# Performance work log

Hardware: AMD Instinct MI355X
Metric: run time of the kernel (lower is better)

## Reference

```python
import jax, jax.numpy as jnp
import numpy as np

B, CIN, L = 4, 128, 2048
D_MODEL, D_STATE, EXPAND, HEADDIM, NGROUPS = 256, 16, 3, 3, 1
D_INNER = EXPAND * D_MODEL            # 768
NHEADS = D_INNER // HEADDIM           # 256
CONV_DIM = D_INNER + 2 * NGROUPS * D_STATE   # 800
D_IN_PROJ = 2 * D_INNER + 2 * NGROUPS * D_STATE + NHEADS  # 1824
K_PROJ, D_CONV = 4, 4
EPS = 1e-5


def setup_inputs() -> dict:
    key = jax.random.key(0)
    ks = jax.random.split(key, 9)
    x = jax.random.normal(ks[0], (B, CIN, L), jnp.float32)
    proj_w = jax.random.normal(ks[1], (D_MODEL, CIN, K_PROJ), jnp.float32) / np.float32(np.sqrt(CIN * K_PROJ))
    in_proj_w = jax.random.normal(ks[2], (D_IN_PROJ, D_MODEL), jnp.float32) / np.float32(np.sqrt(D_MODEL))
    conv_w = jax.random.normal(ks[3], (CONV_DIM, 1, D_CONV), jnp.float32) / np.float32(np.sqrt(D_CONV))
    conv_b = jax.random.normal(ks[4], (CONV_DIM,), jnp.float32) * 0.01
    # dt_bias = inverse-softplus of dt ~ LogUniform[1e-3, 1e-1] (mamba2 init)
    u = jax.random.uniform(ks[5], (NHEADS,), jnp.float32)
    dt = jnp.exp(u * np.float32(np.log(0.1) - np.log(1e-3)) + np.float32(np.log(1e-3)))
    dt_bias = dt + jnp.log(-jnp.expm1(-dt))
    A_log = jnp.log(1.0 + 15.0 * jax.random.uniform(ks[6], (NHEADS,), jnp.float32))  # A in [-16,-1]
    D_skip = jnp.ones((NHEADS,), jnp.float32)
    norm_w = jnp.ones((D_INNER,), jnp.float32)
    out_proj_w = jax.random.normal(ks[7], (D_MODEL, D_INNER), jnp.float32) / np.float32(np.sqrt(D_INNER))
    return {"x": x, "proj_w": proj_w, "in_proj_w": in_proj_w, "conv_w": conv_w,
            "conv_b": conv_b, "dt_bias": dt_bias, "A_log": A_log, "D_skip": D_skip,
            "norm_w": norm_w, "out_proj_w": out_proj_w}


def _forward(x, proj_w, in_proj_w, conv_w, conv_b, dt_bias, A_log, D_skip, norm_w, out_proj_w):
    # outer Conv1d, padding='same' (k=4 -> left 1, right 2), no bias: (B,CIN,L)->(B,D_MODEL,L)
    h = jax.lax.conv_general_dilated(x, proj_w, (1,), [(1, 2)],
                                     dimension_numbers=("NCH", "OIH", "NCH"))
    u = h.transpose(0, 2, 1)                          # (B, L, d_model)
    zxbcdt = jnp.einsum("bld,ed->ble", u, in_proj_w)  # (B, L, 1824)
    z = zxbcdt[..., :D_INNER]                                     # (B,L,768)
    xBC = zxbcdt[..., D_INNER:D_INNER + CONV_DIM]                 # (B,L,800)
    dt = zxbcdt[..., D_INNER + CONV_DIM:]                         # (B,L,256)
    dt = jax.nn.softplus(dt + dt_bias)
    # depthwise causal conv (pad d_conv-1 on left) + SiLU
    xBC_c = jax.lax.conv_general_dilated(xBC.transpose(0, 2, 1), conv_w, (1,), [(D_CONV - 1, 0)],
                                         feature_group_count=CONV_DIM,
                                         dimension_numbers=("NCH", "OIH", "NCH"))
    xBC = jax.nn.silu(xBC_c + conv_b[None, :, None]).transpose(0, 2, 1)  # (B,L,800)
    xs = xBC[..., :D_INNER].reshape(B, L, NHEADS, HEADDIM)        # (B,L,H,P)
    Bm = xBC[..., D_INNER:D_INNER + D_STATE]                      # (B,L,N) (ngroups=1)
    Cm = xBC[..., D_INNER + D_STATE:]                             # (B,L,N)
    A = -jnp.exp(A_log)                                           # (H,)

    def step(hst, inp):
        dt_t, x_t, B_t, C_t = inp                 # (B,H),(B,H,P),(B,N),(B,N)
        dA = jnp.exp(dt_t * A)[:, :, None, None]  # (B,H,1,1)
        hst = dA * hst + jnp.einsum("bh,bhp,bn->bhpn", dt_t, x_t, B_t)
        y_t = jnp.einsum("bhpn,bn->bhp", hst, C_t)
        return hst, y_t

    h0 = jnp.zeros((B, NHEADS, HEADDIM, D_STATE), x.dtype)
    _, ys = jax.lax.scan(step, h0, (dt.transpose(1, 0, 2), xs.transpose(1, 0, 2, 3),
                                    Bm.transpose(1, 0, 2), Cm.transpose(1, 0, 2)))
    y = ys.transpose(1, 0, 2, 3) + D_skip[None, None, :, None] * xs   # (B,L,H,P)
    y = y.reshape(B, L, D_INNER)
    # gated RMSNorm: gate first, then normalize (norm_before_gate=False)
    y = y * jax.nn.silu(z)
    y = y * jax.lax.rsqrt(jnp.mean(y * y, axis=-1, keepdims=True) + EPS) * norm_w
    out = jnp.einsum("ble,de->bld", y, out_proj_w)   # (B,L,d_model)
    return out.transpose(0, 2, 1)                    # (B,d_model,L)


def reference(x, proj_w, in_proj_w, conv_w, conv_b, dt_bias, A_log, D_skip, norm_w, out_proj_w):
    return _forward(x, proj_w, in_proj_w, conv_w, conv_b, dt_bias, A_log, D_skip, norm_w, out_proj_w)
```

## Files before the change

### kernel.cpp

```cpp
#include <hip/hip_runtime.h>
#include <hip/hip_fp16.h>
#include <math.h>

#define B_     4
#define CIN    128
#define LEN    2048
#define DMODEL 256
#define DSTATE 16
#define NHEADS 256
#define DINNER 768
#define CONVDIM 800
#define DINPROJ 1824
#define EPS_   1e-5f
#define BAND   64
#define NBAND  32

typedef _Float16 f16x8 __attribute__((ext_vector_type(8)));
typedef _Float16 f16x4 __attribute__((ext_vector_type(4)));
typedef float    f32x4 __attribute__((ext_vector_type(4)));

__device__ __forceinline__ float silu_(float x){ return x / (1.0f + __expf(-x)); }
__device__ __forceinline__ float softplus_(float x){
    return x > 0.f ? x + log1pf(__expf(-x)) : log1pf(__expf(x));
}

__device__ __forceinline__ void gl2lds16(const _Float16* g, _Float16* l){
    __builtin_amdgcn_global_load_lds(
        (const __attribute__((address_space(1))) void*)g,
        (__attribute__((address_space(3))) void*)l, 16, 0, 0);
}

__global__ __launch_bounds__(256) void k_f2h(const float* __restrict__ a,
                                             _Float16* __restrict__ o, int n){
    for (int i = blockIdx.x * 256 + threadIdx.x; i < n; i += gridDim.x * 256)
        o[i] = (_Float16)a[i];
}

__global__ __launch_bounds__(256) void k_im2col(const float* __restrict__ x,
                                                _Float16* __restrict__ xcol){
    __shared__ float xs[CIN][68];
    int blk = blockIdx.x;
    int b  = blk >> 5;
    int l0 = (blk & 31) << 6;
    const float* xb = x + (size_t)b * CIN * LEN;
    for (int idx = threadIdx.x; idx < CIN * 67; idx += 256){
        int ci = idx / 67, j = idx % 67;
        int gl = l0 - 1 + j;
        xs[ci][j] = (gl >= 0 && gl < LEN) ? xb[ci * LEN + gl] : 0.f;
    }
    __syncthreads();
    #pragma unroll
    for (int v = 0; v < 16; v++){
        int id = v * 256 + threadIdx.x;
        int rl = id >> 6, c = id & 63;
        f16x8 pk;
        #pragma unroll
        for (int e = 0; e < 8; e++){
            int ci = c * 2 + (e >> 2), k = e & 3;
            pk[e] = (_Float16)xs[ci][rl + k];
        }
        *(f16x8*)&xcol[((size_t)(b * LEN + l0 + rl)) * 512 + c * 8] = pk;
    }
}

template<int K, int EPI>
__global__ __launch_bounds__(256) void k_gemm(const _Float16* __restrict__ A,
                                              const _Float16* __restrict__ Bw,
                                              const float* __restrict__ dt_bias,
                                              _Float16* __restrict__ o_u,
                                              _Float16* __restrict__ o_z,
                                              _Float16* __restrict__ o_xbc,
                                              _Float16* __restrict__ o_dt,
                                              float* __restrict__ o_f){
    __shared__ __align__(16) _Float16 As[128 * 32];
    __shared__ __align__(16) _Float16 Bs[128 * 32];
    int tid  = threadIdx.x;
    int wv   = tid >> 6;
    int lane = tid & 63;
    int quad = lane >> 4;
    int l16  = lane & 15;
    int m0 = blockIdx.x * 128;
    int n0 = blockIdx.y * 128;
    int wm = (wv >> 1) * 64;
    int wn = (wv & 1) * 64;
    int srow = lane >> 2;
    int scol = (lane & 3) * 8;

    f32x4 acc[4][4];
    #pragma unroll
    for (int i = 0; i < 4; i++)
        #pragma unroll
        for (int j = 0; j < 4; j++)
            acc[i][j] = (f32x4){0.f, 0.f, 0.f, 0.f};

    for (int k0 = 0; k0 < K; k0 += 32){
        #pragma unroll
        for (int j = 0; j < 2; j++){
            int ar = m0 + wv * 32 + j * 16 + srow;
            gl2lds16(A + (size_t)ar * K + k0 + scol,
                     &As[(wv * 32 + j * 16) * 32]);
            int nr = n0 + wv * 32 + j * 16 + srow;
            if (EPI == 1) nr = nr > (DINPROJ - 1) ? (DINPROJ - 1) : nr;
            gl2lds16(Bw + (size_t)nr * K + k0 + scol,
                     &Bs[(wv * 32 + j * 16) * 32]);
        }
        __syncthreads();
        f16x8 af[4], bf[4];
        #pragma unroll
        for (int i = 0; i < 4; i++)
            af[i] = *(const f16x8*)&As[(wm + i * 16 + l16) * 32 + quad * 8];
        #pragma unroll
        for (int j = 0; j < 4; j++)
            bf[j] = *(const f16x8*)&Bs[(wn + j * 16 + l16) * 32 + quad * 8];
        #pragma unroll
        for (int i = 0; i < 4; i++)
            #pragma unroll
            for (int j = 0; j < 4; j++)
                acc[i][j] = __builtin_amdgcn_mfma_f32_16x16x32_f16(
                                af[i], bf[j], acc[i][j], 0, 0, 0);
        __syncthreads();
    }

    if (EPI == 0){
        #pragma unroll
        for (int j = 0; j < 4; j++){
            int col = n0 + wn + j * 16 + l16;
            #pragma unroll
            for (int i = 0; i < 4; i++){
                int row = m0 + wm + i * 16 + quad * 4;
                #pragma unroll
                for (int r = 0; r < 4; r++)
                    o_u[(size_t)(row + r) * DMODEL + col] = (_Float16)acc[i][j][r];
            }
        }
    } else if (EPI == 1){
        #pragma unroll
        for (int j = 0; j < 4; j++){
            int col = n0 + wn + j * 16 + l16;
            if (col < DINNER){
                #pragma unroll
                for (int i = 0; i < 4; i++){
                    int row = m0 + wm + i * 16 + quad * 4;
                    #pragma unroll
                    for (int r = 0; r < 4; r++)
                        o_z[(size_t)(row + r) * DINNER + col] = (_Float16)acc[i][j][r];
                }
            } else if (col < DINNER + CONVDIM){
                int cc = col - DINNER;
                #pragma unroll
                for (int i = 0; i < 4; i++){
                    int row = m0 + wm + i * 16 + quad * 4;
                    #pragma unroll
                    for (int r = 0; r < 4; r++)
                        o_xbc[(size_t)(row + r) * CONVDIM + cc] = (_Float16)acc[i][j][r];
                }
            } else if (col < DINPROJ){
                int hh = col - (DINNER + CONVDIM);
                float bias = dt_bias[hh];
                #pragma unroll
                for (int i = 0; i < 4; i++){
                    int row = m0 + wm + i * 16 + quad * 4;
                    #pragma unroll
                    for (int r = 0; r < 4; r++)
                        o_dt[(size_t)(row + r) * NHEADS + hh] =
                            (_Float16)softplus_(acc[i][j][r] + bias);
                }
            }
        }
    } else {
        #pragma unroll
        for (int i = 0; i < 4; i++){
            int row = m0 + wm + i * 16 + quad * 4;
            int b = row >> 11, l = row & (LEN - 1);
            #pragma unroll
            for (int j = 0; j < 4; j++){
                int d = n0 + wn + j * 16 + l16;
                *(f32x4*)&o_f[(((size_t)(b * DMODEL + d)) << 11) + l] = acc[i][j];
            }
        }
    }
}

__global__ __launch_bounds__(256) void k_dwconv(const __half* __restrict__ xbc,
                                                const float* __restrict__ cw,
                                                const float* __restrict__ cb,
                                                __half* __restrict__ xcc){
    int idx = blockIdx.x * 256 + threadIdx.x;
    int c = idx % CONVDIM;
    int r = idx / CONVDIM;
    int l = r & (LEN - 1);
    float4 wv = *(const float4*)(cw + c * 4);
    float acc = cb[c];
    if (l >= 3){
        const __half* base = xbc + (size_t)(r - 3) * CONVDIM + c;
        acc += __half2float(base[0]) * wv.x + __half2float(base[CONVDIM]) * wv.y +
               __half2float(base[2 * CONVDIM]) * wv.z + __half2float(base[3 * CONVDIM]) * wv.w;
    } else {
        const float wk[4] = {wv.x, wv.y, wv.z, wv.w};
        for (int k = 0; k < 4; k++){
            int t = l - 3 + k;
            if (t >= 0) acc += __half2float(xbc[(size_t)(r + k - 3) * CONVDIM + c]) * wk[k];
        }
    }
    xcc[idx] = __float2half(silu_(acc));
}

__global__ __launch_bounds__(256, 3) void k_y(const __half* __restrict__ dtb,
                                              const __half* __restrict__ xcc,
                                              const float* __restrict__ A_log,
                                              __half* __restrict__ y,
                                              float* __restrict__ E0,
                                              __half* __restrict__ cstate,
                                              float* __restrict__ dsum){
    __shared__ __align__(16) char smem[45056];
    __half* sBC = (__half*)smem;
    __half* sX  = (__half*)(smem + 5120);
    float*  sG  = (float*)(smem + 18432);
    float*  sD  = (float*)(smem + 22528);
    __half* sDT = (__half*)(smem + 31744);
    __half* sHL = (__half*)(smem + 35840);

    int band = blockIdx.x, hg = blockIdx.y, b = blockIdx.z;
    int row0 = band * BAND;
    int tid = threadIdx.x;
    int wv = tid >> 6, lane = tid & 63;

    {
        int row = tid >> 2, off = tid & 3;
        f16x8 v = *(const f16x8*)((const char*)xcc +
                    (size_t)(b * LEN + row0 + row) * 1600 + 1536 + off * 16);
        *(f16x8*)&sBC[row * 40 + off * 8] = v;
    }
    #pragma unroll
    for (int i = 0; i < 3; i++){
        int c = tid + i * 256;
        int row = c / 12, off = c % 12;
        f16x8 v = *(const f16x8*)((const char*)xcc +
                    (size_t)(b * LEN + row0 + row) * 1600 + hg * 192 + off * 16);
        *(f16x8*)&sX[row * 104 + off * 8] = v;
    }
    gl2lds16((const _Float16*)((const char*)dtb +
               (size_t)(b * LEN + row0 + (tid >> 2)) * 512 + hg * 64 + (lane & 3) * 16),
             (_Float16*)(smem + 31744 + wv * 1024));
    __syncthreads();

    {
        int h = tid & 31;
        float A = -__expf(A_log[hg * 32 + h]);
        #pragma unroll
        for (int i = 0; i < 8; i++){
            int t = (tid >> 5) + i * 8;
            sD[t * 36 + h] = __expf(A * __half2float(sDT[t * 32 + h]));
        }
    }
    __syncthreads();

    if (tid < 32){
        int h = tid;
        float E = 1.f;
        float* ep = E0 + ((size_t)(b * LEN + row0)) * 256 + hg * 32 + h;
        for (int t = 0; t < 64; t++){
            E *= sD[t * 36 + h];
            *ep = E;
            ep += 256;
        }
        dsum[(size_t)(b * 256 + hg * 32 + h) * NBAND + band] = E;
    } else if (tid < 160){
        int base = (tid - 32) * 8;
        int tt = base >> 4;
        f16x8 ca = *(const f16x8*)&sBC[tt * 40 + 16];
        f16x8 cb = *(const f16x8*)&sBC[tt * 40 + 24];
        float cf[16];
        #pragma unroll
        for (int n = 0; n < 16; n++) cf[n] = (n < 8) ? (float)ca[n] : (float)cb[n - 8];
        #pragma unroll
        for (int j = 0; j < 8; j++){
            int idx = base + j;
            int t2 = idx >> 4, ss = idx & 15;
            if (t2 != tt){
                tt = t2;
                ca = *(const f16x8*)&sBC[tt * 40 + 16];
                cb = *(const f16x8*)&sBC[tt * 40 + 24];
                #pragma unroll
                for (int n = 0; n < 16; n++) cf[n] = (n < 8) ? (float)ca[n] : (float)cb[n - 8];
            }
            int s = (tt & 48) + ss;
            f16x8 ba = *(const f16x8*)&sBC[s * 40];
            f16x8 bb = *(const f16x8*)&sBC[s * 40 + 8];
            float acc = 0.f;
            #pragma unroll
            for (int n = 0; n < 8; n++)
                acc += cf[n] * (float)ba[n] + cf[n + 8] * (float)bb[n];
            sG[tt * 16 + ss] = acc;
        }
    } else {
        for (int idx = tid - 160; idx < 2048; idx += 96){
            int t = idx >> 5, h = idx & 31;
            float dtv = __half2float(sDT[t * 32 + h]);
            int xi = t * 104 + h * 3;
            sX[xi]     = (_Float16)((float)sX[xi]     * dtv);
            sX[xi + 1] = (_Float16)((float)sX[xi + 1] * dtv);
            sX[xi + 2] = (_Float16)((float)sX[xi + 2] * dtv);
        }
    }
    __syncthreads();

    int t = tid >> 2, hsub = tid & 3, Hb = hsub * 8;
    int tmod = t & 15, tseg = t & 48;
    float w[8], y0[8], y1[8], y2[8];
    #pragma unroll
    for (int i = 0; i < 8; i++){ w[i] = 1.f; y0[i] = 0.f; y1[i] = 0.f; y2[i] = 0.f; }

    for (int d = 0; d <= tmod; d++){
        int s = t - d;
        float g = sG[t * 16 + (tmod - d)];
        f32x4 Dv0 = *(const f32x4*)&sD[s * 36 + Hb];
        f32x4 Dv1 = *(const f32x4*)&sD[s * 36 + Hb + 4];
        f16x8 xv0 = *(const f16x8*)&sX[s * 104 + hsub * 24];
        f16x8 xv1 = *(const f16x8*)&sX[s * 104 + hsub * 24 + 8];
        f16x8 xv2 = *(const f16x8*)&sX[s * 104 + hsub * 24 + 16];
        #define XV(i) ((i) < 8 ? (float)xv0[(i)] : ((i) < 16 ? (float)xv1[(i)-8] : (float)xv2[(i)-16]))
        #pragma unroll
        for (int hh = 0; hh < 8; hh++){
            float wg = w[hh] * g;
            y0[hh] = fmaf(wg, XV(hh * 3 + 0), y0[hh]);
            y1[hh] = fmaf(wg, XV(hh * 3 + 1), y1[hh]);
            y2[hh] = fmaf(wg, XV(hh * 3 + 2), y2[hh]);
            w[hh] *= (hh < 4) ? Dv0[hh] : Dv1[hh - 4];
        }
        #undef XV
    }

    if (tid < 128){
        int h2 = tid >> 2, ng = tid & 3;
        float hc[12];
        #pragma unroll
        for (int i = 0; i < 12; i++) hc[i] = 0.f;
        for (int k = 0; k < 4; k++){
            float F[12];
            #pragma unroll
            for (int i = 0; i < 12; i++) F[i] = 0.f;
            float v = 1.f;
            for (int ss = 15; ss >= 0; ss--){
                int s = k * 16 + ss;
                float x0 = (float)sX[s * 104 + h2 * 3];
                float x1 = (float)sX[s * 104 + h2 * 3 + 1];
                float x2 = (float)sX[s * 104 + h2 * 3 + 2];
                f16x4 bv = *(const f16x4*)&sBC[s * 40 + ng * 4];
                #pragma unroll
                for (int nn = 0; nn < 4; nn++){
                    float wb = v * (float)bv[nn];
                    F[nn * 3 + 0] = fmaf(wb, x0, F[nn * 3 + 0]);
                    F[nn * 3 + 1] = fmaf(wb, x1, F[nn * 3 + 1]);
                    F[nn * 3 + 2] = fmaf(wb, x2, F[nn * 3 + 2]);
                }
                v *= sD[s * 36 + h2];
            }
            #pragma unroll
            for (int i = 0; i < 12; i++) hc[i] = fmaf(v, hc[i], F[i]);
            if (k < 3){
                __half* hp = &sHL[(k * 32 + h2) * 48 + ng * 12];
                #pragma unroll
                for (int q = 0; q < 3; q++){
                    f16x4 pk;
                    #pragma unroll
                    for (int e = 0; e < 4; e++) pk[e] = (_Float16)hc[q * 4 + e];
                    *(f16x4*)&hp[q * 4] = pk;
                }
            } else {
                __half* cp = cstate + ((size_t)((b * 256 + hg * 32 + h2) * NBAND + band)) * 48 + ng * 12;
                #pragma unroll
                for (int q = 0; q < 3; q++){
                    f16x4 pk;
                    #pragma unroll
                    for (int e = 0; e < 4; e++) pk[e] = (_Float16)hc[q * 4 + e];
                    *(f16x4*)&cp[q * 4] = pk;
                }
            }
        }
    }
    __syncthreads();

    {
        f16x8 cva = *(const f16x8*)&sBC[t * 40 + 16];
        f16x8 cvb = *(const f16x8*)&sBC[t * 40 + 24];
        float cf[16];
        #pragma unroll
        for (int n = 0; n < 16; n++) cf[n] = (n < 8) ? (float)cva[n] : (float)cvb[n - 8];
        int k = t >> 4;
        if (k > 0){
            #pragma unroll
            for (int hh = 0; hh < 8; hh++){
                int h = Hb + hh;
                const __half* hl = &sHL[((k - 1) * 32 + h) * 48];
                f16x8 hv0 = *(const f16x8*)&hl[0];
                f16x8 hv1 = *(const f16x8*)&hl[8];
                f16x8 hv2 = *(const f16x8*)&hl[16];
                f16x8 hv3 = *(const f16x8*)&hl[24];
                f16x8 hv4 = *(const f16x8*)&hl[32];
                f16x8 hv5 = *(const f16x8*)&hl[40];
                #define HV(i) ((i)<8?(float)hv0[(i)]:(i)<16?(float)hv1[(i)-8]:(i)<24?(float)hv2[(i)-16]:\
                               (i)<32?(float)hv3[(i)-24]:(i)<40?(float)hv4[(i)-32]:(float)hv5[(i)-40])
                float a0 = 0.f, a1 = 0.f, a2 = 0.f;
                #pragma unroll
                for (int n = 0; n < 16; n++){
                    a0 = fmaf(cf[n], HV(n * 3 + 0), a0);
                    a1 = fmaf(cf[n], HV(n * 3 + 1), a1);
                    a2 = fmaf(cf[n], HV(n * 3 + 2), a2);
                }
                #undef HV
                y0[hh] = fmaf(w[hh], a0, y0[hh]);
                y1[hh] = fmaf(w[hh], a1, y1[hh]);
                y2[hh] = fmaf(w[hh], a2, y2[hh]);
            }
        }
        __half* yp = y + (size_t)(b * LEN + row0 + t) * DINNER + hg * 96 + hsub * 24;
        #pragma unroll
        for (int c = 0; c < 3; c++){
            f16x8 pk;
            #pragma unroll
            for (int e2 = 0; e2 < 8; e2++){
                int gi = c * 8 + e2;
                int hh = gi / 3, p = gi % 3;
                pk[e2] = (_Float16)(p == 0 ? y0[hh] : (p == 1 ? y1[hh] : y2[hh]));
            }
            *(f16x8*)&yp[c * 8] = pk;
        }
    }
}

__global__ __launch_bounds__(64) void k_scanB(__half* __restrict__ cstate,
                                              const float* __restrict__ dsum){
    int bh = blockIdx.x;
    int lane = threadIdx.x;
    if (lane >= 48) return;
    __half* st = cstate + (size_t)bh * NBAND * 48 + lane;
    const float* dd = dsum + (size_t)bh * NBAND;
    float H = 0.f;
    for (int c = 0; c < NBAND; c++){
        float d = dd[c];
        float s = __half2float(st[(size_t)c * 48]);
        st[(size_t)c * 48] = __float2half(H);
        H = fmaf(H, d, s);
    }
}

__global__ __launch_bounds__(256) void k_norm(__half* __restrict__ y,
                                              const __half* __restrict__ z,
                                              const __half* __restrict__ xcc,
                                              const float* __restrict__ E0,
                                              const __half* __restrict__ cstate,
                                              const float* __restrict__ D_skip,
                                              const float* __restrict__ nw){
    __shared__ __align__(16) char nsm[24576 + 64];
    __half* sHI = (__half*)nsm;
    float*  sCf = (float*)(nsm + 24576);
    __shared__ float wsum[4];
    int r = blockIdx.x;
    int b = r >> 11, l = r & (LEN - 1), band = l >> 6;
    int tid = threadIdx.x;
    int wv = tid >> 6, lane = tid & 63;

    #pragma unroll
    for (int i = 0; i < 6; i++){
        int chunk = (wv + i * 4) * 64 + lane;
        int head = chunk / 6, off = chunk % 6;
        gl2lds16((const _Float16*)((const char*)cstate +
                   ((size_t)(b * 256 + head) * NBAND + band) * 96 + off * 16),
                 (_Float16*)(nsm + (wv + i * 4) * 1024));
    }
    if (tid < 16)
        sCf[tid] = __half2float(xcc[(size_t)r * CONVDIM + DINNER + DSTATE + tid]);
    __syncthreads();

    const __half* zr = z + (size_t)r * DINNER;
    const __half* xr = xcc + (size_t)r * CONVDIM;
    const float*  er = E0 + (size_t)r * 256;
    __half* yr = y + (size_t)r * DINNER;
    float tv[3];
    #pragma unroll
    for (int q = 0; q < 3; q++){
        int e = tid + q * 256;
        int h = e / 3, p = e - h * 3;
        float corr = 0.f;
        #pragma unroll
        for (int n = 0; n < 16; n++)
            corr = fmaf(sCf[n], __half2float(sHI[h * 48 + n * 3 + p]), corr);
        float yf = __half2float(yr[e]) + er[h] * corr + D_skip[h] * __half2float(xr[e]);
        tv[q] = yf * silu_(__half2float(zr[e]));
    }
    float ss = tv[0] * tv[0] + tv[1] * tv[1] + tv[2] * tv[2];
    #pragma unroll
    for (int m = 1; m < 64; m <<= 1) ss += __shfl_xor(ss, m, 64);
    if ((tid & 63) == 0) wsum[tid >> 6] = ss;
    __syncthreads();
    float tot = wsum[0] + wsum[1] + wsum[2] + wsum[3];
    float sc = rsqrtf(tot / (float)DINNER + EPS_);
    #pragma unroll
    for (int q = 0; q < 3; q++){
        int e = tid + q * 256;
        yr[e] = __float2half(tv[q] * sc * nw[e]);
    }
}

extern "C" void kernel_launch(void* const* d_in, const int* in_sizes, int n_in,
                              void* d_out, int out_size, void* d_ws, size_t ws_size,
                              hipStream_t stream) {
    const float* x          = (const float*)d_in[0];
    const float* proj_w     = (const float*)d_in[1];
    const float* in_proj_w  = (const float*)d_in[2];
    const float* conv_w     = (const float*)d_in[3];
    const float* conv_b     = (const float*)d_in[4];
    const float* dt_bias    = (const float*)d_in[5];
    const float* A_log      = (const float*)d_in[6];
    const float* D_skip     = (const float*)d_in[7];
    const float* norm_w     = (const float*)d_in[8];
    const float* out_proj_w = (const float*)d_in[9];
    float* out = (float*)d_out;

    char* ob = (char*)d_out;
    _Float16* pw_h  = (_Float16*)ob;
    _Float16* ipw_h = (_Float16*)(ob + 262144);
    float*    E0    = (float*)d_out;

    char* wsb = (char*)d_ws;
    _Float16* xcol  = (_Float16*)(wsb);
    _Float16* u_h   = (_Float16*)(wsb + 8388608);
    __half*   xcc_h = (__half*)(wsb);
    __half*   z_h   = (__half*)(wsb + 13107200);
    __half*   xbc_h = (__half*)(wsb + 25690112);
    __half*   y_h   = xbc_h;
    __half*   dt_h  = (__half*)(wsb + 38797312);
    __half*   cstate= (__half*)(wsb + 42991616);
    float*    dsum  = (float*)(wsb + 46137344);
    _Float16* opw_h = (_Float16*)(wsb + 46268416);

    k_f2h   <<<64, 256, 0, stream>>>(proj_w,     pw_h,  DMODEL * CIN * 4);
    k_f2h   <<<64, 256, 0, stream>>>(in_proj_w,  ipw_h, DINPROJ * DMODEL);
    k_f2h   <<<64, 256, 0, stream>>>(out_proj_w, opw_h, DMODEL * DINNER);
    k_im2col<<<128, 256, 0, stream>>>(x, xcol);
    k_gemm<512, 0><<<dim3(64, 2), 256, 0, stream>>>(xcol, pw_h, nullptr,
        u_h, nullptr, nullptr, nullptr, nullptr);
    k_gemm<256, 1><<<dim3(64, 15), 256, 0, stream>>>(u_h, ipw_h, dt_bias,
        nullptr, (_Float16*)z_h, (_Float16*)xbc_h, (_Float16*)dt_h, nullptr);
    k_dwconv<<<25600, 256, 0, stream>>>(xbc_h, conv_w, conv_b, xcc_h);
    k_y     <<<dim3(NBAND, 8, B_), 256, 0, stream>>>(dt_h, xcc_h, A_log,
                                                     y_h, E0, cstate, dsum);
    k_scanB <<<1024, 64, 0, stream>>>(cstate, dsum);
    k_norm  <<<8192, 256, 0, stream>>>(y_h, z_h, xcc_h, E0, cstate, D_skip, norm_w);
    k_gemm<768, 2><<<dim3(64, 2), 256, 0, stream>>>((const _Float16*)y_h, opw_h,
        nullptr, nullptr, nullptr, nullptr, nullptr, out);
}
```

Before: 326.5 us.

## Relayout y, E0 and chunk states into head-group panels for contiguous access

The scan kernel now writes y and E0 in per-head-group panels (32 heads, 96 channels) so each block's stores are contiguous. Chunk states and decay sums move to a band-major layout, so the normalization kernel loads a band's states with simple contiguous 16-byte chunks instead of strided per-head gathers. The normalization output now goes in place into the z buffer, which feeds the output projection. The cost is strided gathers from the panel layout in k_norm and a more strided sequential scan in k_scanB.

```diff
diff --git a/kernel.cpp b/kernel.cpp
--- a/kernel.cpp
+++ b/kernel.cpp
@@ -258,13 +258,13 @@
     if (tid < 32){
         int h = tid;
         float E = 1.f;
-        float* ep = E0 + ((size_t)(b * LEN + row0)) * 256 + hg * 32 + h;
+        float* ep = E0 + ((size_t)(hg * (B_ * LEN) + b * LEN + row0)) * 32 + h;
         for (int t = 0; t < 64; t++){
             E *= sD[t * 36 + h];
             *ep = E;
-            ep += 256;
-        }
-        dsum[(size_t)(b * 256 + hg * 32 + h) * NBAND + band] = E;
+            ep += 32;
+        }
+        dsum[(size_t)((b * NBAND + band) * 256) + hg * 32 + h] = E;
     } else if (tid < 160){
         int base = (tid - 32) * 8;
         int tt = base >> 4;
@@ -306,7 +306,7 @@
     __syncthreads();
 
     int t = tid >> 2, hsub = tid & 3, Hb = hsub * 8;
-    int tmod = t & 15, tseg = t & 48;
+    int tmod = t & 15;
     float w[8], y0[8], y1[8], y2[8];
     #pragma unroll
     for (int i = 0; i < 8; i++){ w[i] = 1.f; y0[i] = 0.f; y1[i] = 0.f; y2[i] = 0.f; }
@@ -368,7 +368,7 @@
                     *(f16x4*)&hp[q * 4] = pk;
                 }
             } else {
-                __half* cp = cstate + ((size_t)((b * 256 + hg * 32 + h2) * NBAND + band)) * 48 + ng * 12;
+                __half* cp = cstate + ((size_t)((b * NBAND + band) * 256 + hg * 32 + h2)) * 48 + ng * 12;
                 #pragma unroll
                 for (int q = 0; q < 3; q++){
                     f16x4 pk;
@@ -414,7 +414,7 @@
                 y2[hh] = fmaf(w[hh], a2, y2[hh]);
             }
         }
-        __half* yp = y + (size_t)(b * LEN + row0 + t) * DINNER + hg * 96 + hsub * 24;
+        __half* yp = y + ((size_t)(hg * (B_ * LEN) + b * LEN + row0 + t)) * 96 + hsub * 24;
         #pragma unroll
         for (int c = 0; c < 3; c++){
             f16x8 pk;
@@ -432,21 +432,23 @@
 __global__ __launch_bounds__(64) void k_scanB(__half* __restrict__ cstate,
                                               const float* __restrict__ dsum){
     int bh = blockIdx.x;
+    int b = bh >> 8, h = bh & 255;
     int lane = threadIdx.x;
     if (lane >= 48) return;
-    __half* st = cstate + (size_t)bh * NBAND * 48 + lane;
-    const float* dd = dsum + (size_t)bh * NBAND;
+    __half* st = cstate + ((size_t)(b * NBAND) * 256 + h) * 48 + lane;
+    const float* dd = dsum + (size_t)(b * NBAND) * 256 + h;
     float H = 0.f;
     for (int c = 0; c < NBAND; c++){
-        float d = dd[c];
-        float s = __half2float(st[(size_t)c * 48]);
-        st[(size_t)c * 48] = __float2half(H);
+        float d = dd[(size_t)c * 256];
+        float s = __half2float(st[(size_t)c * 256 * 48]);
+        st[(size_t)c * 256 * 48] = __float2half(H);
         H = fmaf(H, d, s);
     }
 }
 
-__global__ __launch_bounds__(256) void k_norm(__half* __restrict__ y,
+__global__ __launch_bounds__(256) void k_norm(const __half* __restrict__ y,
                                               const __half* __restrict__ z,
+                                              __half* __restrict__ zy,
                                               const __half* __restrict__ xcc,
                                               const float* __restrict__ E0,
                                               const __half* __restrict__ cstate,
@@ -461,13 +463,12 @@
     int tid = threadIdx.x;
     int wv = tid >> 6, lane = tid & 63;
 
+    const char* cbase = (const char*)cstate + ((size_t)(b * NBAND + band) * 256) * 96;
     #pragma unroll
     for (int i = 0; i < 6; i++){
-        int chunk = (wv + i * 4) * 64 + lane;
-        int head = chunk / 6, off = chunk % 6;
-        gl2lds16((const _Float16*)((const char*)cstate +
-                   ((size_t)(b * 256 + head) * NBAND + band) * 96 + off * 16),
-                 (_Float16*)(nsm + (wv + i * 4) * 1024));
+        int chunk = wv + i * 4;
+        gl2lds16((const _Float16*)(cbase + (size_t)chunk * 1024 + lane * 16),
+                 (_Float16*)(nsm + chunk * 1024));
     }
     if (tid < 16)
         sCf[tid] = __half2float(xcc[(size_t)r * CONVDIM + DINNER + DSTATE + tid]);
@@ -475,8 +476,7 @@
 
     const __half* zr = z + (size_t)r * DINNER;
     const __half* xr = xcc + (size_t)r * CONVDIM;
-    const float*  er = E0 + (size_t)r * 256;
-    __half* yr = y + (size_t)r * DINNER;
+    __half* zyr = zy + (size_t)r * DINNER;
     float tv[3];
     #pragma unroll
     for (int q = 0; q < 3; q++){
@@ -486,7 +486,10 @@
         #pragma unroll
         for (int n = 0; n < 16; n++)
             corr = fmaf(sCf[n], __half2float(sHI[h * 48 + n * 3 + p]), corr);
-        float yf = __half2float(yr[e]) + er[h] * corr + D_skip[h] * __half2float(xr[e]);
+        size_t pbase = (size_t)((h >> 5) * (B_ * LEN)) + r;
+        float ypan = __half2float(y[pbase * 96 + (h & 31) * 3 + p]);
+        float e0   = E0[pbase * 32 + (h & 31)];
+        float yf = ypan + e0 * corr + D_skip[h] * __half2float(xr[e]);
         tv[q] = yf * silu_(__half2float(zr[e]));
     }
     float ss = tv[0] * tv[0] + tv[1] * tv[1] + tv[2] * tv[2];
@@ -499,7 +502,7 @@
     #pragma unroll
     for (int q = 0; q < 3; q++){
         int e = tid + q * 256;
-        yr[e] = __float2half(tv[q] * sc * nw[e]);
+        zyr[e] = __float2half(tv[q] * sc * nw[e]);
     }
 }
 
@@ -547,7 +550,8 @@
     k_y     <<<dim3(NBAND, 8, B_), 256, 0, stream>>>(dt_h, xcc_h, A_log,
                                                      y_h, E0, cstate, dsum);
     k_scanB <<<1024, 64, 0, stream>>>(cstate, dsum);
-    k_norm  <<<8192, 256, 0, stream>>>(y_h, z_h, xcc_h, E0, cstate, D_skip, norm_w);
-    k_gemm<768, 2><<<dim3(64, 2), 256, 0, stream>>>((const _Float16*)y_h, opw_h,
+    k_norm  <<<8192, 256, 0, stream>>>(y_h, z_h, z_h, xcc_h, E0, cstate,
+                                       D_skip, norm_w);
+    k_gemm<768, 2><<<dim3(64, 2), 256, 0, stream>>>((const _Float16*)z_h, opw_h,
         nullptr, nullptr, nullptr, nullptr, nullptr, out);
 }
```

After: 330.1 us. About the same (+1.1%).

## Widen k_y head group to 64 heads per block with async LDS loads

Applied to the files above, without the earlier changes.

The chunked-scan kernel now handles 64 heads per block instead of 32, halving the grid in the head dimension. The shared B/C and G computations are amortised over twice as many heads. All global-to-LDS staging goes through the direct gl2lds16 path, and the LDS layout is repacked without padding, with sHL aliasing the sX buffer. Every thread now computes the per-chunk state partials in registers, not just half of them. This doubles per-thread accumulators (16 heads × 4 arrays), which raises register pressure and reduces occupancy, and with fewer blocks the GPU may be less filled.

```diff
diff --git a/kernel.cpp b/kernel.cpp
--- a/kernel.cpp
+++ b/kernel.cpp
@@ -205,194 +205,195 @@
     xcc[idx] = __float2half(silu_(acc));
 }
 
-__global__ __launch_bounds__(256, 3) void k_y(const __half* __restrict__ dtb,
-                                              const __half* __restrict__ xcc,
-                                              const float* __restrict__ A_log,
-                                              __half* __restrict__ y,
-                                              float* __restrict__ E0,
-                                              __half* __restrict__ cstate,
-                                              float* __restrict__ dsum){
-    __shared__ __align__(16) char smem[45056];
+__global__ __launch_bounds__(256) void k_y(const __half* __restrict__ dtb,
+                                           const __half* __restrict__ xcc,
+                                           const float* __restrict__ A_log,
+                                           __half* __restrict__ y,
+                                           float* __restrict__ E0,
+                                           __half* __restrict__ cstate,
+                                           float* __restrict__ dsum){
+    __shared__ __align__(16) char smem[59392];
     __half* sBC = (__half*)smem;
-    __half* sX  = (__half*)(smem + 5120);
-    float*  sG  = (float*)(smem + 18432);
-    float*  sD  = (float*)(smem + 22528);
-    __half* sDT = (__half*)(smem + 31744);
-    __half* sHL = (__half*)(smem + 35840);
-
-    int band = blockIdx.x, hg = blockIdx.y, b = blockIdx.z;
+    __half* sX  = (__half*)(smem + 4096);
+    __half* sHL = (__half*)(smem + 4096);
+    __half* sDT = (__half*)(smem + 28672);
+    float*  sD  = (float*)(smem + 36864);
+    float*  sG  = (float*)(smem + 54272);
+
+    int band = blockIdx.x, hq = blockIdx.y, b = blockIdx.z;
     int row0 = band * BAND;
     int tid = threadIdx.x;
     int wv = tid >> 6, lane = tid & 63;
 
     {
-        int row = tid >> 2, off = tid & 3;
-        f16x8 v = *(const f16x8*)((const char*)xcc +
-                    (size_t)(b * LEN + row0 + row) * 1600 + 1536 + off * 16);
-        *(f16x8*)&sBC[row * 40 + off * 8] = v;
-    }
-    #pragma unroll
-    for (int i = 0; i < 3; i++){
-        int c = tid + i * 256;
-        int row = c / 12, off = c % 12;
-        f16x8 v = *(const f16x8*)((const char*)xcc +
-                    (size_t)(b * LEN + row0 + row) * 1600 + hg * 192 + off * 16);
-        *(f16x8*)&sX[row * 104 + off * 8] = v;
-    }
-    gl2lds16((const _Float16*)((const char*)dtb +
-               (size_t)(b * LEN + row0 + (tid >> 2)) * 512 + hg * 64 + (lane & 3) * 16),
-             (_Float16*)(smem + 31744 + wv * 1024));
+        int c = wv, slot = c * 64 + lane;
+        int row = slot >> 2, off = slot & 3;
+        gl2lds16((const _Float16*)((const char*)xcc +
+                   (size_t)(b * LEN + row0 + row) * 1600 + 1536 + off * 16),
+                 (_Float16*)(smem + c * 1024));
+    }
+    #pragma unroll
+    for (int i = 0; i < 6; i++){
+        int c = wv + i * 4, slot = c * 64 + lane;
+        int row = slot / 24, off = slot % 24;
+        gl2lds16((const _Float16*)((const char*)xcc +
+                   (size_t)(b * LEN + row0 + row) * 1600 + hq * 384 + off * 16),
+                 (_Float16*)(smem + 4096 + c * 1024));
+    }
+    #pragma unroll
+    for (int i = 0; i < 2; i++){
+        int c = wv + i * 4, slot = c * 64 + lane;
+        int row = slot >> 3, off = slot & 7;
+        gl2lds16((const _Float16*)((const char*)dtb +
+                   (size_t)(b * LEN + row0 + row) * 512 + hq * 128 + off * 16),
+                 (_Float16*)(smem + 28672 + c * 1024));
+    }
     __syncthreads();
 
     {
-        int h = tid & 31;
-        float A = -__expf(A_log[hg * 32 + h]);
-        #pragma unroll
-        for (int i = 0; i < 8; i++){
-            int t = (tid >> 5) + i * 8;
-            sD[t * 36 + h] = __expf(A * __half2float(sDT[t * 32 + h]));
-        }
-    }
-    __syncthreads();
-
-    if (tid < 32){
+        int h = tid & 63, tb = tid >> 6;
+        float A = -__expf(A_log[hq * 64 + h]);
+        #pragma unroll
+        for (int i = 0; i < 16; i++){
+            int t = tb + i * 4;
+            sD[t * 68 + h] = __expf(A * __half2float(sDT[t * 64 + h]));
+        }
+    }
+    __syncthreads();
+
+    if (tid < 64){
         int h = tid;
         float E = 1.f;
-        float* ep = E0 + ((size_t)(b * LEN + row0)) * 256 + hg * 32 + h;
+        float* ep = E0 + ((size_t)(b * LEN + row0)) * 256 + hq * 64 + h;
         for (int t = 0; t < 64; t++){
-            E *= sD[t * 36 + h];
+            E *= sD[t * 68 + h];
             *ep = E;
             ep += 256;
         }
-        dsum[(size_t)(b * 256 + hg * 32 + h) * NBAND + band] = E;
-    } else if (tid < 160){
-        int base = (tid - 32) * 8;
-        int tt = base >> 4;
-        f16x8 ca = *(const f16x8*)&sBC[tt * 40 + 16];
-        f16x8 cb = *(const f16x8*)&sBC[tt * 40 + 24];
+        dsum[(size_t)(b * 256 + hq * 64 + h) * NBAND + band] = E;
+    } else if (tid < 128){
+        int tt = tid - 64;
+        f16x8 ca = *(const f16x8*)&sBC[tt * 32 + 16];
+        f16x8 cb = *(const f16x8*)&sBC[tt * 32 + 24];
         float cf[16];
         #pragma unroll
         for (int n = 0; n < 16; n++) cf[n] = (n < 8) ? (float)ca[n] : (float)cb[n - 8];
-        #pragma unroll
-        for (int j = 0; j < 8; j++){
-            int idx = base + j;
-            int t2 = idx >> 4, ss = idx & 15;
-            if (t2 != tt){
-                tt = t2;
-                ca = *(const f16x8*)&sBC[tt * 40 + 16];
-                cb = *(const f16x8*)&sBC[tt * 40 + 24];
-                #pragma unroll
-                for (int n = 0; n < 16; n++) cf[n] = (n < 8) ? (float)ca[n] : (float)cb[n - 8];
-            }
+        for (int ss = 0; ss < 16; ss++){
             int s = (tt & 48) + ss;
-            f16x8 ba = *(const f16x8*)&sBC[s * 40];
-            f16x8 bb = *(const f16x8*)&sBC[s * 40 + 8];
+            f16x8 ba = *(const f16x8*)&sBC[s * 32];
+            f16x8 bb = *(const f16x8*)&sBC[s * 32 + 8];
             float acc = 0.f;
             #pragma unroll
             for (int n = 0; n < 8; n++)
                 acc += cf[n] * (float)ba[n] + cf[n + 8] * (float)bb[n];
-            sG[tt * 16 + ss] = acc;
+            sG[tt * 20 + ss] = acc;
         }
     } else {
-        for (int idx = tid - 160; idx < 2048; idx += 96){
-            int t = idx >> 5, h = idx & 31;
-            float dtv = __half2float(sDT[t * 32 + h]);
-            int xi = t * 104 + h * 3;
-            sX[xi]     = (_Float16)((float)sX[xi]     * dtv);
-            sX[xi + 1] = (_Float16)((float)sX[xi + 1] * dtv);
-            sX[xi + 2] = (_Float16)((float)sX[xi + 2] * dtv);
-        }
-    }
-    __syncthreads();
-
-    int t = tid >> 2, hsub = tid & 3, Hb = hsub * 8;
-    int tmod = t & 15, tseg = t & 48;
-    float w[8], y0[8], y1[8], y2[8];
-    #pragma unroll
-    for (int i = 0; i < 8; i++){ w[i] = 1.f; y0[i] = 0.f; y1[i] = 0.f; y2[i] = 0.f; }
+        for (int idx = tid - 128; idx < 4096; idx += 128){
+            int t = idx >> 6, h = idx & 63;
+            float dtv = __half2float(sDT[t * 64 + h]);
+            int xi = t * 192 + h * 3;
+            sX[xi]     = __float2half(__half2float(sX[xi])     * dtv);
+            sX[xi + 1] = __float2half(__half2float(sX[xi + 1]) * dtv);
+            sX[xi + 2] = __float2half(__half2float(sX[xi + 2]) * dtv);
+        }
+    }
+    __syncthreads();
+
+    int t = tid >> 2, hsub = tid & 3, Hb = hsub * 16;
+    int tmod = t & 15;
+    float w[16], y0[16], y1[16], y2[16];
+    #pragma unroll
+    for (int i = 0; i < 16; i++){ w[i] = 1.f; y0[i] = 0.f; y1[i] = 0.f; y2[i] = 0.f; }
 
     for (int d = 0; d <= tmod; d++){
         int s = t - d;
-        float g = sG[t * 16 + (tmod - d)];
-        f32x4 Dv0 = *(const f32x4*)&sD[s * 36 + Hb];
-        f32x4 Dv1 = *(const f32x4*)&sD[s * 36 + Hb + 4];
-        f16x8 xv0 = *(const f16x8*)&sX[s * 104 + hsub * 24];
-        f16x8 xv1 = *(const f16x8*)&sX[s * 104 + hsub * 24 + 8];
-        f16x8 xv2 = *(const f16x8*)&sX[s * 104 + hsub * 24 + 16];
-        #define XV(i) ((i) < 8 ? (float)xv0[(i)] : ((i) < 16 ? (float)xv1[(i)-8] : (float)xv2[(i)-16]))
-        #pragma unroll
-        for (int hh = 0; hh < 8; hh++){
+        float g = sG[t * 20 + (tmod - d)];
+        f32x4 Dv[4];
+        #pragma unroll
+        for (int k4 = 0; k4 < 4; k4++)
+            Dv[k4] = *(const f32x4*)&sD[s * 68 + Hb + k4 * 4];
+        f16x8 xv0 = *(const f16x8*)&sX[s * 192 + Hb * 3];
+        f16x8 xv1 = *(const f16x8*)&sX[s * 192 + Hb * 3 + 8];
+        f16x8 xv2 = *(const f16x8*)&sX[s * 192 + Hb * 3 + 16];
+        f16x8 xv3 = *(const f16x8*)&sX[s * 192 + Hb * 3 + 24];
+        f16x8 xv4 = *(const f16x8*)&sX[s * 192 + Hb * 3 + 32];
+        f16x8 xv5 = *(const f16x8*)&sX[s * 192 + Hb * 3 + 40];
+        #define XV(i) ((i)<8?(float)xv0[(i)]:(i)<16?(float)xv1[(i)-8]:(i)<24?(float)xv2[(i)-16]:\
+                       (i)<32?(float)xv3[(i)-24]:(i)<40?(float)xv4[(i)-32]:(float)xv5[(i)-40])
+        #pragma unroll
+        for (int hh = 0; hh < 16; hh++){
             float wg = w[hh] * g;
             y0[hh] = fmaf(wg, XV(hh * 3 + 0), y0[hh]);
             y1[hh] = fmaf(wg, XV(hh * 3 + 1), y1[hh]);
             y2[hh] = fmaf(wg, XV(hh * 3 + 2), y2[hh]);
-            w[hh] *= (hh < 4) ? Dv0[hh] : Dv1[hh - 4];
+            w[hh] *= Dv[hh >> 2][hh & 3];
         }
         #undef XV
     }
 
-    if (tid < 128){
-        int h2 = tid >> 2, ng = tid & 3;
+    int h2 = tid >> 2, ng = tid & 3;
+    float F[4][12];
+    float vK[4];
+    #pragma unroll
+    for (int k = 0; k < 4; k++){
+        #pragma unroll
+        for (int i = 0; i < 12; i++) F[k][i] = 0.f;
+        float v = 1.f;
+        for (int ss = 15; ss >= 0; ss--){
+            int s = k * 16 + ss;
+            float x0 = __half2float(sX[s * 192 + h2 * 3]);
+            float x1 = __half2float(sX[s * 192 + h2 * 3 + 1]);
+            float x2 = __half2float(sX[s * 192 + h2 * 3 + 2]);
+            f16x4 bv = *(const f16x4*)&sBC[s * 32 + ng * 4];
+            #pragma unroll
+            for (int nn = 0; nn < 4; nn++){
+                float wb = v * (float)bv[nn];
+                F[k][nn * 3 + 0] = fmaf(wb, x0, F[k][nn * 3 + 0]);
+                F[k][nn * 3 + 1] = fmaf(wb, x1, F[k][nn * 3 + 1]);
+                F[k][nn * 3 + 2] = fmaf(wb, x2, F[k][nn * 3 + 2]);
+            }
+            v *= sD[s * 68 + h2];
+        }
+        vK[k] = v;
+    }
+
+    __syncthreads();
+
+    {
         float hc[12];
         #pragma unroll
-        for (int i = 0; i < 12; i++) hc[i] = 0.f;
-        for (int k = 0; k < 4; k++){
-            float F[12];
-            #pragma unroll
-            for (int i = 0; i < 12; i++) F[i] = 0.f;
-            float v = 1.f;
-            for (int ss = 15; ss >= 0; ss--){
-                int s = k * 16 + ss;
-                float x0 = (float)sX[s * 104 + h2 * 3];
-                float x1 = (float)sX[s * 104 + h2 * 3 + 1];
-                float x2 = (float)sX[s * 104 + h2 * 3 + 2];
-                f16x4 bv = *(const f16x4*)&sBC[s * 40 + ng * 4];
-                #pragma unroll
-                for (int nn = 0; nn < 4; nn++){
-                    float wb = v * (float)bv[nn];
-                    F[nn * 3 + 0] = fmaf(wb, x0, F[nn * 3 + 0]);
-                    F[nn * 3 + 1] = fmaf(wb, x1, F[nn * 3 + 1]);
-                    F[nn * 3 + 2] = fmaf(wb, x2, F[nn * 3 + 2]);
-                }
-                v *= sD[s * 36 + h2];
-            }
-            #pragma unroll
-            for (int i = 0; i < 12; i++) hc[i] = fmaf(v, hc[i], F[i]);
-            if (k < 3){
-                __half* hp = &sHL[(k * 32 + h2) * 48 + ng * 12];
-                #pragma unroll
-                for (int q = 0; q < 3; q++){
-                    f16x4 pk;
-                    #pragma unroll
-                    for (int e = 0; e < 4; e++) pk[e] = (_Float16)hc[q * 4 + e];
-                    *(f16x4*)&hp[q * 4] = pk;
-                }
-            } else {
-                __half* cp = cstate + ((size_t)((b * 256 + hg * 32 + h2) * NBAND + band)) * 48 + ng * 12;
-                #pragma unroll
-                for (int q = 0; q < 3; q++){
-                    f16x4 pk;
-                    #pragma unroll
-                    for (int e = 0; e < 4; e++) pk[e] = (_Float16)hc[q * 4 + e];
-                    *(f16x4*)&cp[q * 4] = pk;
-                }
-            }
-        }
+        for (int i = 0; i < 12; i++) hc[i] = F[0][i];
+        #pragma unroll
+        for (int i = 0; i < 12; i++)
+            sHL[(0 * 64 + h2) * 48 + ng * 12 + i] = __float2half(hc[i]);
+        #pragma unroll
+        for (int k = 1; k <= 2; k++){
+            #pragma unroll
+            for (int i = 0; i < 12; i++) hc[i] = fmaf(vK[k], hc[i], F[k][i]);
+            #pragma unroll
+            for (int i = 0; i < 12; i++)
+                sHL[(k * 64 + h2) * 48 + ng * 12 + i] = __float2half(hc[i]);
+        }
+        __half* cp = cstate + ((size_t)((b * 256 + hq * 64 + h2) * NBAND + band)) * 48 + ng * 12;
+        #pragma unroll
+        for (int i = 0; i < 12; i++)
+            cp[i] = __float2half(fmaf(vK[3], hc[i], F[3][i]));
     }
     __syncthreads();
 
     {
-        f16x8 cva = *(const f16x8*)&sBC[t * 40 + 16];
-        f16x8 cvb = *(const f16x8*)&sBC[t * 40 + 24];
+        f16x8 cva = *(const f16x8*)&sBC[t * 32 + 16];
+        f16x8 cvb = *(const f16x8*)&sBC[t * 32 + 24];
         float cf[16];
         #pragma unroll
         for (int n = 0; n < 16; n++) cf[n] = (n < 8) ? (float)cva[n] : (float)cvb[n - 8];
         int k = t >> 4;
         if (k > 0){
             #pragma unroll
-            for (int hh = 0; hh < 8; hh++){
+            for (int hh = 0; hh < 16; hh++){
                 int h = Hb + hh;
-                const __half* hl = &sHL[((k - 1) * 32 + h) * 48];
+                const __half* hl = &sHL[((k - 1) * 64 + h) * 48];
                 f16x8 hv0 = *(const f16x8*)&hl[0];
                 f16x8 hv1 = *(const f16x8*)&hl[8];
                 f16x8 hv2 = *(const f16x8*)&hl[16];
@@ -414,9 +415,9 @@
                 y2[hh] = fmaf(w[hh], a2, y2[hh]);
             }
         }
-        __half* yp = y + (size_t)(b * LEN + row0 + t) * DINNER + hg * 96 + hsub * 24;
-        #pragma unroll
-        for (int c = 0; c < 3; c++){
+        __half* yp = y + (size_t)(b * LEN + row0 + t) * DINNER + hq * 192 + hsub * 48;
+        #pragma unroll
+        for (int c = 0; c < 6; c++){
             f16x8 pk;
             #pragma unroll
             for (int e2 = 0; e2 < 8; e2++){
@@ -544,10 +545,11 @@
     k_gemm<256, 1><<<dim3(64, 15), 256, 0, stream>>>(u_h, ipw_h, dt_bias,
         nullptr, (_Float16*)z_h, (_Float16*)xbc_h, (_Float16*)dt_h, nullptr);
     k_dwconv<<<25600, 256, 0, stream>>>(xbc_h, conv_w, conv_b, xcc_h);
-    k_y     <<<dim3(NBAND, 8, B_), 256, 0, stream>>>(dt_h, xcc_h, A_log,
+    k_y     <<<dim3(NBAND, 4, B_), 256, 0, stream>>>(dt_h, xcc_h, A_log,
                                                      y_h, E0, cstate, dsum);
     k_scanB <<<1024, 64, 0, stream>>>(cstate, dsum);
-    k_norm  <<<8192, 256, 0, stream>>>(y_h, z_h, xcc_h, E0, cstate, D_skip, norm_w);
+    k_norm  <<<8192, 256, 0, stream>>>(y_h, z_h, xcc_h, E0, cstate,
+                                       D_skip, norm_w);
     k_gemm<768, 2><<<dim3(64, 2), 256, 0, stream>>>((const _Float16*)y_h, opw_h,
         nullptr, nullptr, nullptr, nullptr, nullptr, out);
 }
```

Result: faster. 289.2 us (-11.4%).
